# Kernel tuning notes

Measured on AMD Instinct MI355X. Metric: run time of the kernel, lower is better.

Reference implementation:

```python
import jax, jax.numpy as jnp
import numpy as np

BZ, D_IN, D_STATE, D_OUT, L = 8, 256, 512, 256, 4096


def setup_inputs() -> dict:
    key = jax.random.key(0)
    k_u, k_a, k_b, k_c = jax.random.split(key, 4)
    init_scale = 0.5
    u = jax.random.normal(k_u, (BZ, D_IN, L), dtype=jnp.float32)
    A_unconstrained = jax.random.normal(k_a, (D_STATE,), dtype=jnp.float32) * 0.1
    B_mat = jax.random.normal(k_b, (D_STATE, D_IN), dtype=jnp.float32) * init_scale / np.sqrt(D_IN)
    C_mat = jax.random.normal(k_c, (D_OUT, D_STATE), dtype=jnp.float32) * init_scale / np.sqrt(D_STATE)
    D_mat = jnp.zeros((D_OUT, D_IN), dtype=jnp.float32)
    h0 = jnp.zeros((D_STATE,), dtype=jnp.float32)
    return {"u": u, "A_unconstrained": A_unconstrained, "B_mat": B_mat,
            "C_mat": C_mat, "D_mat": D_mat, "h0": h0}


def reference(u, A_unconstrained, B_mat, C_mat, D_mat, h0):
    # u: (B, input_dim, L)
    Bz = u.shape[0]
    A_diag = -jax.nn.softplus(A_unconstrained)          # (S,)
    # Precompute input projection for all timesteps: (L, B, S)
    Bu = jnp.einsum('bil,si->lbs', u, B_mat)
    state0 = jnp.broadcast_to(h0[None, :], (Bz, A_diag.shape[0]))

    def step(state, bu_t):
        x_t = state * A_diag[None, :] + bu_t            # (B, S)
        return x_t, x_t

    _, xs = jax.lax.scan(step, state0, Bu)              # xs: (L, B, S)
    # y_t = x_t @ C^T + u_t @ D^T, assembled as (B, output_dim, L)
    Y = jnp.einsum('lbs,os->bol', xs, C_mat) + jnp.einsum('bil,oi->bol', u, D_mat)
    return Y
```

## Files before the change

### kernel.cpp

```cpp
#include <hip/hip_runtime.h>
#include <math.h>

#define BZ 8
#define DI 256
#define DS 512
#define DOUT 256
#define LL 4096
#define BS (BZ * DS)
#define CH 64
#define CT 64
#define TST 136

typedef __bf16 bf16x8 __attribute__((ext_vector_type(8)));
typedef float f32x4 __attribute__((ext_vector_type(4)));
typedef unsigned short us8 __attribute__((ext_vector_type(8)));

__device__ __forceinline__ ushort f2b(float f) {
    union { float f; unsigned u; } v; v.f = f;
    unsigned r = v.u + 0x7FFFu + ((v.u >> 16) & 1u);
    return (ushort)(r >> 16);
}
__device__ __forceinline__ float b2f(ushort h) {
    union { unsigned u; float f; } v; v.u = ((unsigned)h) << 16;
    return v.f;
}

__device__ __forceinline__ void gload16(const ushort* g, ushort* l) {
    __builtin_amdgcn_global_load_lds(
        (const __attribute__((address_space(1))) unsigned int*)g,
        (__attribute__((address_space(3))) unsigned int*)l,
        16, 0, 0);
}

__global__ __launch_bounds__(256) void k_prep(const float* __restrict__ Au,
                                              float* __restrict__ apow,
                                              const float* __restrict__ Bm,
                                              const float* __restrict__ Cm,
                                              const float* __restrict__ Dm,
                                              ushort* __restrict__ Bmb,
                                              ushort* __restrict__ Cmb,
                                              ushort* __restrict__ Dmb,
                                              int* __restrict__ dflag) {
    const int t = blockIdx.x * 256 + threadIdx.x;
    const int n1 = DS * DI / 4, n2 = DOUT * DS / 4, n3 = DOUT * DI / 4;
    if (t < n1) {
        float4 v = ((const float4*)Bm)[t];
        ushort4 o; o.x = f2b(v.x); o.y = f2b(v.y); o.z = f2b(v.z); o.w = f2b(v.w);
        ((ushort4*)Bmb)[t] = o;
    } else if (t < n1 + n2) {
        float4 v = ((const float4*)Cm)[t - n1];
        ushort4 o; o.x = f2b(v.x); o.y = f2b(v.y); o.z = f2b(v.z); o.w = f2b(v.w);
        ((ushort4*)Cmb)[t - n1] = o;
    } else if (t < n1 + n2 + n3) {
        float4 v = ((const float4*)Dm)[t - n1 - n2];
        ushort4 o; o.x = f2b(v.x); o.y = f2b(v.y); o.z = f2b(v.z); o.w = f2b(v.w);
        ((ushort4*)Dmb)[t - n1 - n2] = o;
        if (v.x != 0.f || v.y != 0.f || v.z != 0.f || v.w != 0.f)
            atomicOr(dflag, 1);
    }
    if (t < DS) {
        float x = Au[t];
        float sp = (x > 15.f) ? x : log1pf(expf(x));
        float ad = -sp;
        float p = 1.f;
        apow[t] = 1.f;
        for (int j = 1; j <= CT; ++j) { p *= ad; apow[j * DS + t] = p; }
    }
}

__global__ __launch_bounds__(256) void k_u2t(const float* __restrict__ u,
                                             ushort* __restrict__ utr) {
    __shared__ float T[64][65];
    const int tid = threadIdx.x;
    const int l0 = blockIdx.x * 64, i0 = blockIdx.y * 64, b = blockIdx.z;
    const int r = tid >> 4, c4 = tid & 15;
#pragma unroll
    for (int rr = r; rr < 64; rr += 16) {
        float4 v = *(const float4*)&u[((size_t)b * DI + i0 + rr) * LL + l0 + c4 * 4];
        T[rr][c4 * 4 + 0] = v.x; T[rr][c4 * 4 + 1] = v.y;
        T[rr][c4 * 4 + 2] = v.z; T[rr][c4 * 4 + 3] = v.w;
    }
    __syncthreads();
#pragma unroll
    for (int ll = r; ll < 64; ll += 16) {
        ushort4 o;
        o.x = f2b(T[c4 * 4 + 0][ll]); o.y = f2b(T[c4 * 4 + 1][ll]);
        o.z = f2b(T[c4 * 4 + 2][ll]); o.w = f2b(T[c4 * 4 + 3][ll]);
        *(ushort4*)&utr[((size_t)b * LL + l0 + ll) * DI + i0 + c4 * 4] = o;
    }
}

__global__ __launch_bounds__(256) void k_bu(const ushort* __restrict__ Bmb,
                                            const ushort* __restrict__ utr,
                                            ushort* __restrict__ Xb,
                                            float* __restrict__ finals,
                                            const float* __restrict__ apow) {
    __shared__ ushort smem[128 * TST];
    const int tid = threadIdx.x;
    const int w = tid >> 6, lane = tid & 63;
    const int l0 = blockIdx.x * 128, s0 = blockIdx.y * 128, b = blockIdx.z;
    const int wm = w & 1, wn = w >> 1;
    const int mrow = lane & 15, quad = lane >> 4;
    const int sr = lane >> 2, sc = (lane & 3) * 8;
    const int off0 = (16 * w) * 32, off1 = (16 * w + 64) * 32;

    f32x4 acc[4][4];
#pragma unroll
    for (int mi = 0; mi < 4; ++mi)
#pragma unroll
        for (int ni = 0; ni < 4; ++ni) acc[mi][ni] = (f32x4)0.f;

    const ushort* ag0 = Bmb + (size_t)(s0 + 16 * w + sr) * DI + sc;
    const ushort* ag1 = ag0 + (size_t)64 * DI;
    const ushort* bg0 = utr + ((size_t)b * LL + l0 + 16 * w + sr) * DI + sc;
    const ushort* bg1 = bg0 + (size_t)64 * DI;

    gload16(ag0, smem + off0); gload16(ag1, smem + off1);
    gload16(bg0, smem + 8192 + off0); gload16(bg1, smem + 8192 + off1);

    for (int it = 0; it < DI / 32; ++it) {
        __syncthreads();
        const int cb = (it & 1) * 4096, nb = 4096 - cb;
        if (it + 1 < DI / 32) {
            const int kk = (it + 1) * 32;
            gload16(ag0 + kk, smem + nb + off0); gload16(ag1 + kk, smem + nb + off1);
            gload16(bg0 + kk, smem + 8192 + nb + off0); gload16(bg1 + kk, smem + 8192 + nb + off1);
        }
        bf16x8 af[4], bfr[4];
#pragma unroll
        for (int mi = 0; mi < 4; ++mi)
            af[mi] = *(const bf16x8*)&smem[cb + (wm * 64 + mi * 16 + mrow) * 32 + quad * 8];
#pragma unroll
        for (int ni = 0; ni < 4; ++ni)
            bfr[ni] = *(const bf16x8*)&smem[8192 + cb + (wn * 64 + ni * 16 + mrow) * 32 + quad * 8];
#pragma unroll
        for (int mi = 0; mi < 4; ++mi)
#pragma unroll
            for (int ni = 0; ni < 4; ++ni)
                acc[mi][ni] = __builtin_amdgcn_mfma_f32_16x16x32_bf16(af[mi], bfr[ni], acc[mi][ni], 0, 0, 0);
    }
    __syncthreads();

#pragma unroll
    for (int mi = 0; mi < 4; ++mi) {
        const int sloc = wm * 64 + mi * 16 + quad * 4;
#pragma unroll
        for (int ni = 0; ni < 4; ++ni) {
            const int lloc = wn * 64 + ni * 16 + mrow;
            f32x4 v = acc[mi][ni];
            ushort4 o; o.x = f2b(v[0]); o.y = f2b(v[1]); o.z = f2b(v[2]); o.w = f2b(v[3]);
            *(ushort4*)&smem[lloc * TST + sloc] = o;
        }
    }
    __syncthreads();
    {
        const int cloc = tid >> 7, sl = tid & 127;
        const float a = apow[DS + s0 + sl];
        float acc2 = 0.f;
        ushort* p = &smem[(cloc * 64) * TST + sl];
#pragma unroll 8
        for (int j = 0; j < CT; ++j) {
            acc2 = a * acc2 + b2f(*p);
            *p = f2b(acc2);
            p += TST;
        }
        finals[(size_t)(l0 / 64 + cloc) * BS + (size_t)b * DS + s0 + sl] = acc2;
    }
    __syncthreads();
    {
        const int rr = tid >> 4, cc = tid & 15;
#pragma unroll
        for (int rep = 0; rep < 8; ++rep) {
            const int l = rep * 16 + rr;
            us8 v = *(const us8*)&smem[l * TST + cc * 8];
            *(us8*)&Xb[(size_t)(l0 + l) * BS + (size_t)b * DS + s0 + cc * 8] = v;
        }
    }
}

__global__ __launch_bounds__(256) void k_carry(const float* __restrict__ finals,
                                               float* __restrict__ carries,
                                               const float* __restrict__ apow,
                                               const float* __restrict__ h0) {
    const int bs = blockIdx.x * 256 + threadIdx.x;
    const int s = bs & (DS - 1);
    const float aT = apow[CT * DS + s];
    float carry = h0[s];
#pragma unroll 8
    for (int c = 0; c < CH; ++c) {
        carries[(size_t)c * BS + bs] = carry;
        carry = aT * carry + finals[(size_t)c * BS + bs];
    }
}

__global__ __launch_bounds__(256) void k_out(const ushort* __restrict__ Cmb,
                                             const ushort* __restrict__ Dmb,
                                             const ushort* __restrict__ Xb,
                                             const ushort* __restrict__ utr,
                                             const float* __restrict__ carries,
                                             const float* __restrict__ apow,
                                             const int* __restrict__ dflag,
                                             float* __restrict__ Y) {
    __shared__ ushort smem[18432];
    const int tid = threadIdx.x;
    const int w = tid >> 6, lane = tid & 63;
    const int l0 = blockIdx.x * 128, o0 = blockIdx.y * 128, b = blockIdx.z;
    const int wm = w & 1, wn = w >> 1;
    const int mrow = lane & 15, quad = lane >> 4;
    const int sr = lane >> 2, sc = (lane & 3) * 8;
    const int off0 = (16 * w) * 32, off1 = (16 * w + 64) * 32;
    const int dnz = *dflag;

    f32x4 acc[4][4];
#pragma unroll
    for (int mi = 0; mi < 4; ++mi)
#pragma unroll
        for (int ni = 0; ni < 4; ++ni) acc[mi][ni] = (f32x4)0.f;

    auto compute = [&](const int aoff, const int ast, const int boff) {
        bf16x8 af[4], bfr[4];
#pragma unroll
        for (int mi = 0; mi < 4; ++mi)
            af[mi] = *(const bf16x8*)&smem[aoff + (wm * 64 + mi * 16 + mrow) * ast + quad * 8];
#pragma unroll
        for (int ni = 0; ni < 4; ++ni)
            bfr[ni] = *(const bf16x8*)&smem[boff + (wn * 64 + ni * 16 + mrow) * 32 + quad * 8];
#pragma unroll
        for (int mi = 0; mi < 4; ++mi)
#pragma unroll
            for (int ni = 0; ni < 4; ++ni)
                acc[mi][ni] = __builtin_amdgcn_mfma_f32_16x16x32_bf16(af[mi], bfr[ni], acc[mi][ni], 0, 0, 0);
    };

    {
        const int r0 = 16 * w + sr;
        const int l_0 = l0 + r0, l_1 = l_0 + 64;
        const int j0 = l_0 & 63, c0 = l_0 >> 6;
        const int j1 = l_1 & 63, c1 = l_1 >> 6;
        const float* ap0 = &apow[(size_t)(j0 + 1) * DS];
        const float* ap1 = &apow[(size_t)(j1 + 1) * DS];
        const float* cr0 = &carries[(size_t)c0 * BS + (size_t)b * DS];
        const float* cr1 = &carries[(size_t)c1 * BS + (size_t)b * DS];
        const ushort* x0 = Xb + (size_t)l_0 * BS + (size_t)b * DS;
        const ushort* x1 = Xb + (size_t)l_1 * BS + (size_t)b * DS;
        const ushort* bg0 = Cmb + (size_t)(o0 + r0) * DS + sc;
        const ushort* bg1 = bg0 + (size_t)64 * DS;

        auto stageA = [&](int it, int dstoff) {
            const int col = it * 32 + sc;
            {
                us8 x = *(const us8*)&x0[col];
                float4 pa = *(const float4*)&ap0[col], pb = *(const float4*)&ap0[col + 4];
                float4 ca = *(const float4*)&cr0[col], cb = *(const float4*)&cr0[col + 4];
                us8 o;
                o[0] = f2b(b2f(x[0]) + pa.x * ca.x); o[1] = f2b(b2f(x[1]) + pa.y * ca.y);
                o[2] = f2b(b2f(x[2]) + pa.z * ca.z); o[3] = f2b(b2f(x[3]) + pa.w * ca.w);
                o[4] = f2b(b2f(x[4]) + pb.x * cb.x); o[5] = f2b(b2f(x[5]) + pb.y * cb.y);
                o[6] = f2b(b2f(x[6]) + pb.z * cb.z); o[7] = f2b(b2f(x[7]) + pb.w * cb.w);
                *(us8*)&smem[dstoff + r0 * 40 + sc] = o;
            }
            {
                us8 x = *(const us8*)&x1[col];
                float4 pa = *(const float4*)&ap1[col], pb = *(const float4*)&ap1[col + 4];
                float4 ca = *(const float4*)&cr1[col], cb = *(const float4*)&cr1[col + 4];
                us8 o;
                o[0] = f2b(b2f(x[0]) + pa.x * ca.x); o[1] = f2b(b2f(x[1]) + pa.y * ca.y);
                o[2] = f2b(b2f(x[2]) + pa.z * ca.z); o[3] = f2b(b2f(x[3]) + pa.w * ca.w);
                o[4] = f2b(b2f(x[4]) + pb.x * cb.x); o[5] = f2b(b2f(x[5]) + pb.y * cb.y);
                o[6] = f2b(b2f(x[6]) + pb.z * cb.z); o[7] = f2b(b2f(x[7]) + pb.w * cb.w);
                *(us8*)&smem[dstoff + (r0 + 64) * 40 + sc] = o;
            }
        };

        stageA(0, 0);
        gload16(bg0, smem + 10240 + off0); gload16(bg1, smem + 10240 + off1);

        for (int it = 0; it < DS / 32; ++it) {
            __syncthreads();
            const int ca_ = (it & 1) * 5120, na_ = 5120 - ca_;
            const int cb_ = 10240 + (it & 1) * 4096, nb_ = 10240 + 4096 - (it & 1) * 4096;
            if (it + 1 < DS / 32) {
                const int kk = (it + 1) * 32;
                gload16(bg0 + kk, smem + nb_ + off0); gload16(bg1 + kk, smem + nb_ + off1);
                stageA(it + 1, na_);
            }
            compute(ca_, 40, cb_);
        }
    }
    if (dnz) {
        const ushort* ag0 = utr + ((size_t)b * LL + l0 + 16 * w + sr) * DI + sc;
        const ushort* ag1 = ag0 + (size_t)64 * DI;
        const ushort* bg0 = Dmb + (size_t)(o0 + 16 * w + sr) * DI + sc;
        const ushort* bg1 = bg0 + (size_t)64 * DI;

        __syncthreads();
        gload16(ag0, smem + off0); gload16(ag1, smem + off1);
        gload16(bg0, smem + 10240 + off0); gload16(bg1, smem + 10240 + off1);

        for (int it = 0; it < DI / 32; ++it) {
            __syncthreads();
            const int ca_ = (it & 1) * 5120, na_ = 5120 - ca_;
            const int cb_ = 10240 + (it & 1) * 4096, nb_ = 10240 + 4096 - (it & 1) * 4096;
            if (it + 1 < DI / 32) {
                const int kk = (it + 1) * 32;
                gload16(ag0 + kk, smem + na_ + off0); gload16(ag1 + kk, smem + na_ + off1);
                gload16(bg0 + kk, smem + nb_ + off0); gload16(bg1 + kk, smem + nb_ + off1);
            }
            compute(ca_, 32, cb_);
        }
    }

#pragma unroll
    for (int mi = 0; mi < 4; ++mi) {
        const int l = l0 + wm * 64 + mi * 16 + quad * 4;
#pragma unroll
        for (int ni = 0; ni < 4; ++ni) {
            const int o = o0 + wn * 64 + ni * 16 + mrow;
            *(float4*)&Y[((size_t)b * DOUT + o) * LL + l] = *(float4*)&acc[mi][ni];
        }
    }
}

extern "C" void kernel_launch(void* const* d_in, const int* in_sizes, int n_in,
                              void* d_out, int out_size, void* d_ws, size_t ws_size,
                              hipStream_t stream) {
    const float* u  = (const float*)d_in[0];
    const float* Au = (const float*)d_in[1];
    const float* Bm = (const float*)d_in[2];
    const float* Cm = (const float*)d_in[3];
    const float* Dm = (const float*)d_in[4];
    const float* h0 = (const float*)d_in[5];
    float* Y = (float*)d_out;

    char* p = (char*)d_ws;
    ushort* utr    = (ushort*)p; p += (size_t)BZ * LL * DI * 2;
    ushort* Xb     = (ushort*)p; p += (size_t)LL * BS * 2;
    float* finals  = (float*)p;  p += (size_t)CH * BS * 4;
    float* carries = (float*)p;  p += (size_t)CH * BS * 4;
    float* apow    = (float*)p;  p += (size_t)(CT + 1) * DS * 4;
    ushort* Bmb    = (ushort*)p; p += (size_t)DS * DI * 2;
    ushort* Cmb    = (ushort*)p; p += (size_t)DOUT * DS * 2;
    ushort* Dmb    = (ushort*)p; p += (size_t)DOUT * DI * 2;
    int* dflag     = (int*)p;    p += 16;

    hipMemsetAsync(dflag, 0, 4, stream);
    k_prep<<<dim3(320), 256, 0, stream>>>(Au, apow, Bm, Cm, Dm, Bmb, Cmb, Dmb, dflag);
    k_u2t<<<dim3(LL / 64, DI / 64, BZ), 256, 0, stream>>>(u, utr);
    k_bu<<<dim3(LL / 128, DS / 128, BZ), 256, 0, stream>>>(Bmb, utr, Xb, finals, apow);
    k_carry<<<dim3(BS / 256), 256, 0, stream>>>(finals, carries, apow, h0);
    k_out<<<dim3(LL / 128, DOUT / 128, BZ), 256, 0, stream>>>(Cmb, Dmb, Xb, utr, carries, apow, dflag, Y);
}
```

Before: 145.4 us.

## Fuse prep into transpose kernel and fold carry scan into output kernel

Merges the weight-conversion/apow prep kernel into the u transpose kernel as extra blocks, and removes the separate carry-scan kernel by having each output block recompute its chunk carries from the per-chunk finals into shared memory. This drops two launches and the carries buffer round trip. In exchange, every k_out block redundantly runs a sequential scan of up to 64 chunks over 512 states, which adds latency before the GEMM starts, especially for blocks handling late chunks.

```diff
diff --git a/kernel.cpp b/kernel.cpp
--- a/kernel.cpp
+++ b/kernel.cpp
@@ -32,61 +32,65 @@
         16, 0, 0);
 }
 
-__global__ __launch_bounds__(256) void k_prep(const float* __restrict__ Au,
-                                              float* __restrict__ apow,
-                                              const float* __restrict__ Bm,
-                                              const float* __restrict__ Cm,
-                                              const float* __restrict__ Dm,
-                                              ushort* __restrict__ Bmb,
-                                              ushort* __restrict__ Cmb,
-                                              ushort* __restrict__ Dmb,
-                                              int* __restrict__ dflag) {
-    const int t = blockIdx.x * 256 + threadIdx.x;
-    const int n1 = DS * DI / 4, n2 = DOUT * DS / 4, n3 = DOUT * DI / 4;
-    if (t < n1) {
-        float4 v = ((const float4*)Bm)[t];
-        ushort4 o; o.x = f2b(v.x); o.y = f2b(v.y); o.z = f2b(v.z); o.w = f2b(v.w);
-        ((ushort4*)Bmb)[t] = o;
-    } else if (t < n1 + n2) {
-        float4 v = ((const float4*)Cm)[t - n1];
-        ushort4 o; o.x = f2b(v.x); o.y = f2b(v.y); o.z = f2b(v.z); o.w = f2b(v.w);
-        ((ushort4*)Cmb)[t - n1] = o;
-    } else if (t < n1 + n2 + n3) {
-        float4 v = ((const float4*)Dm)[t - n1 - n2];
-        ushort4 o; o.x = f2b(v.x); o.y = f2b(v.y); o.z = f2b(v.z); o.w = f2b(v.w);
-        ((ushort4*)Dmb)[t - n1 - n2] = o;
-        if (v.x != 0.f || v.y != 0.f || v.z != 0.f || v.w != 0.f)
-            atomicOr(dflag, 1);
-    }
-    if (t < DS) {
-        float x = Au[t];
-        float sp = (x > 15.f) ? x : log1pf(expf(x));
-        float ad = -sp;
-        float p = 1.f;
-        apow[t] = 1.f;
-        for (int j = 1; j <= CT; ++j) { p *= ad; apow[j * DS + t] = p; }
-    }
-}
-
-__global__ __launch_bounds__(256) void k_u2t(const float* __restrict__ u,
-                                             ushort* __restrict__ utr) {
+__global__ __launch_bounds__(256) void k_prep_u2t(const float* __restrict__ u,
+                                                  ushort* __restrict__ utr,
+                                                  const float* __restrict__ Au,
+                                                  float* __restrict__ apow,
+                                                  const float* __restrict__ Bm,
+                                                  const float* __restrict__ Cm,
+                                                  const float* __restrict__ Dm,
+                                                  ushort* __restrict__ Bmb,
+                                                  ushort* __restrict__ Cmb,
+                                                  ushort* __restrict__ Dmb,
+                                                  int* __restrict__ dflag) {
     __shared__ float T[64][65];
     const int tid = threadIdx.x;
-    const int l0 = blockIdx.x * 64, i0 = blockIdx.y * 64, b = blockIdx.z;
-    const int r = tid >> 4, c4 = tid & 15;
-#pragma unroll
-    for (int rr = r; rr < 64; rr += 16) {
-        float4 v = *(const float4*)&u[((size_t)b * DI + i0 + rr) * LL + l0 + c4 * 4];
-        T[rr][c4 * 4 + 0] = v.x; T[rr][c4 * 4 + 1] = v.y;
-        T[rr][c4 * 4 + 2] = v.z; T[rr][c4 * 4 + 3] = v.w;
-    }
-    __syncthreads();
-#pragma unroll
-    for (int ll = r; ll < 64; ll += 16) {
-        ushort4 o;
-        o.x = f2b(T[c4 * 4 + 0][ll]); o.y = f2b(T[c4 * 4 + 1][ll]);
-        o.z = f2b(T[c4 * 4 + 2][ll]); o.w = f2b(T[c4 * 4 + 3][ll]);
-        *(ushort4*)&utr[((size_t)b * LL + l0 + ll) * DI + i0 + c4 * 4] = o;
+    const int id = blockIdx.x;
+    if (id < 2048) {
+        const int l0 = (id & 63) * 64;
+        const int i0 = ((id >> 6) & 3) * 64;
+        const int b  = id >> 8;
+        const int r = tid >> 4, c4 = tid & 15;
+#pragma unroll
+        for (int rr = r; rr < 64; rr += 16) {
+            float4 v = *(const float4*)&u[((size_t)b * DI + i0 + rr) * LL + l0 + c4 * 4];
+            T[rr][c4 * 4 + 0] = v.x; T[rr][c4 * 4 + 1] = v.y;
+            T[rr][c4 * 4 + 2] = v.z; T[rr][c4 * 4 + 3] = v.w;
+        }
+        __syncthreads();
+#pragma unroll
+        for (int ll = r; ll < 64; ll += 16) {
+            ushort4 o;
+            o.x = f2b(T[c4 * 4 + 0][ll]); o.y = f2b(T[c4 * 4 + 1][ll]);
+            o.z = f2b(T[c4 * 4 + 2][ll]); o.w = f2b(T[c4 * 4 + 3][ll]);
+            *(ushort4*)&utr[((size_t)b * LL + l0 + ll) * DI + i0 + c4 * 4] = o;
+        }
+    } else {
+        const int t = (id - 2048) * 256 + tid;
+        const int n1 = DS * DI / 4, n2 = DOUT * DS / 4, n3 = DOUT * DI / 4;
+        if (t < n1) {
+            float4 v = ((const float4*)Bm)[t];
+            ushort4 o; o.x = f2b(v.x); o.y = f2b(v.y); o.z = f2b(v.z); o.w = f2b(v.w);
+            ((ushort4*)Bmb)[t] = o;
+        } else if (t < n1 + n2) {
+            float4 v = ((const float4*)Cm)[t - n1];
+            ushort4 o; o.x = f2b(v.x); o.y = f2b(v.y); o.z = f2b(v.z); o.w = f2b(v.w);
+            ((ushort4*)Cmb)[t - n1] = o;
+        } else if (t < n1 + n2 + n3) {
+            float4 v = ((const float4*)Dm)[t - n1 - n2];
+            ushort4 o; o.x = f2b(v.x); o.y = f2b(v.y); o.z = f2b(v.z); o.w = f2b(v.w);
+            ((ushort4*)Dmb)[t - n1 - n2] = o;
+            if (v.x != 0.f || v.y != 0.f || v.z != 0.f || v.w != 0.f)
+                atomicOr(dflag, 1);
+        }
+        if (t < DS) {
+            float x = Au[t];
+            float sp = (x > 15.f) ? x : log1pf(expf(x));
+            float ad = -sp;
+            float p = 1.f;
+            apow[t] = 1.f;
+            for (int j = 1; j <= CT; ++j) { p *= ad; apow[j * DS + t] = p; }
+        }
     }
 }
 
@@ -178,30 +182,17 @@
     }
 }
 
-__global__ __launch_bounds__(256) void k_carry(const float* __restrict__ finals,
-                                               float* __restrict__ carries,
-                                               const float* __restrict__ apow,
-                                               const float* __restrict__ h0) {
-    const int bs = blockIdx.x * 256 + threadIdx.x;
-    const int s = bs & (DS - 1);
-    const float aT = apow[CT * DS + s];
-    float carry = h0[s];
-#pragma unroll 8
-    for (int c = 0; c < CH; ++c) {
-        carries[(size_t)c * BS + bs] = carry;
-        carry = aT * carry + finals[(size_t)c * BS + bs];
-    }
-}
-
 __global__ __launch_bounds__(256) void k_out(const ushort* __restrict__ Cmb,
                                              const ushort* __restrict__ Dmb,
                                              const ushort* __restrict__ Xb,
                                              const ushort* __restrict__ utr,
-                                             const float* __restrict__ carries,
+                                             const float* __restrict__ finals,
                                              const float* __restrict__ apow,
+                                             const float* __restrict__ h0,
                                              const int* __restrict__ dflag,
                                              float* __restrict__ Y) {
-    __shared__ ushort smem[18432];
+    __shared__ ushort smem[20480];
+    float* crs = (float*)&smem[18432];
     const int tid = threadIdx.x;
     const int w = tid >> 6, lane = tid & 63;
     const int l0 = blockIdx.x * 128, o0 = blockIdx.y * 128, b = blockIdx.z;
@@ -235,23 +226,35 @@
     {
         const int r0 = 16 * w + sr;
         const int l_0 = l0 + r0, l_1 = l_0 + 64;
-        const int j0 = l_0 & 63, c0 = l_0 >> 6;
-        const int j1 = l_1 & 63, c1 = l_1 >> 6;
+        const int j0 = l_0 & 63;
+        const int j1 = l_1 & 63;
+        const int c0 = l0 >> 6;
         const float* ap0 = &apow[(size_t)(j0 + 1) * DS];
         const float* ap1 = &apow[(size_t)(j1 + 1) * DS];
-        const float* cr0 = &carries[(size_t)c0 * BS + (size_t)b * DS];
-        const float* cr1 = &carries[(size_t)c1 * BS + (size_t)b * DS];
         const ushort* x0 = Xb + (size_t)l_0 * BS + (size_t)b * DS;
         const ushort* x1 = Xb + (size_t)l_1 * BS + (size_t)b * DS;
         const ushort* bg0 = Cmb + (size_t)(o0 + r0) * DS + sc;
         const ushort* bg1 = bg0 + (size_t)64 * DS;
+
+        gload16(bg0, smem + 10240 + off0); gload16(bg1, smem + 10240 + off1);
+
+        for (int s = tid; s < DS; s += 256) {
+            const float aT = apow[CT * DS + s];
+            float carry = h0[s];
+            const float* fb = finals + (size_t)b * DS + s;
+            for (int c = 0; c < c0; ++c)
+                carry = aT * carry + fb[(size_t)c * BS];
+            crs[s] = carry;
+            crs[DS + s] = aT * carry + fb[(size_t)c0 * BS];
+        }
+        __syncthreads();
 
         auto stageA = [&](int it, int dstoff) {
             const int col = it * 32 + sc;
             {
                 us8 x = *(const us8*)&x0[col];
                 float4 pa = *(const float4*)&ap0[col], pb = *(const float4*)&ap0[col + 4];
-                float4 ca = *(const float4*)&cr0[col], cb = *(const float4*)&cr0[col + 4];
+                float4 ca = *(const float4*)&crs[col], cb = *(const float4*)&crs[col + 4];
                 us8 o;
                 o[0] = f2b(b2f(x[0]) + pa.x * ca.x); o[1] = f2b(b2f(x[1]) + pa.y * ca.y);
                 o[2] = f2b(b2f(x[2]) + pa.z * ca.z); o[3] = f2b(b2f(x[3]) + pa.w * ca.w);
@@ -262,7 +265,7 @@
             {
                 us8 x = *(const us8*)&x1[col];
                 float4 pa = *(const float4*)&ap1[col], pb = *(const float4*)&ap1[col + 4];
-                float4 ca = *(const float4*)&cr1[col], cb = *(const float4*)&cr1[col + 4];
+                float4 ca = *(const float4*)&crs[DS + col], cb = *(const float4*)&crs[DS + col + 4];
                 us8 o;
                 o[0] = f2b(b2f(x[0]) + pa.x * ca.x); o[1] = f2b(b2f(x[1]) + pa.y * ca.y);
                 o[2] = f2b(b2f(x[2]) + pa.z * ca.z); o[3] = f2b(b2f(x[3]) + pa.w * ca.w);
@@ -273,7 +276,6 @@
         };
 
         stageA(0, 0);
-        gload16(bg0, smem + 10240 + off0); gload16(bg1, smem + 10240 + off1);
 
         for (int it = 0; it < DS / 32; ++it) {
             __syncthreads();
@@ -336,7 +338,6 @@
     ushort* utr    = (ushort*)p; p += (size_t)BZ * LL * DI * 2;
     ushort* Xb     = (ushort*)p; p += (size_t)LL * BS * 2;
     float* finals  = (float*)p;  p += (size_t)CH * BS * 4;
-    float* carries = (float*)p;  p += (size_t)CH * BS * 4;
     float* apow    = (float*)p;  p += (size_t)(CT + 1) * DS * 4;
     ushort* Bmb    = (ushort*)p; p += (size_t)DS * DI * 2;
     ushort* Cmb    = (ushort*)p; p += (size_t)DOUT * DS * 2;
@@ -344,9 +345,7 @@
     int* dflag     = (int*)p;    p += 16;
 
     hipMemsetAsync(dflag, 0, 4, stream);
-    k_prep<<<dim3(320), 256, 0, stream>>>(Au, apow, Bm, Cm, Dm, Bmb, Cmb, Dmb, dflag);
-    k_u2t<<<dim3(LL / 64, DI / 64, BZ), 256, 0, stream>>>(u, utr);
+    k_prep_u2t<<<dim3(2368), 256, 0, stream>>>(u, utr, Au, apow, Bm, Cm, Dm, Bmb, Cmb, Dmb, dflag);
     k_bu<<<dim3(LL / 128, DS / 128, BZ), 256, 0, stream>>>(Bmb, utr, Xb, finals, apow);
-    k_carry<<<dim3(BS / 256), 256, 0, stream>>>(finals, carries, apow, h0);
-    k_out<<<dim3(LL / 128, DOUT / 128, BZ), 256, 0, stream>>>(Cmb, Dmb, Xb, utr, carries, apow, dflag, Y);
-}
+    k_out<<<dim3(LL / 128, DOUT / 128, BZ), 256, 0, stream>>>(Cmb, Dmb, Xb, utr, finals, apow, h0, dflag, Y);
+}
```

Measured after the change: 160.7 us. 10.5% more time.

## Merge prep and transpose kernels; halve k_out L-tile to 64

Applied to the files above, without the earlier changes.

Fuses the weight-conversion/prep kernel and the u transpose kernel into one launch, dispatching on block index, so one launch and its gap go away. Changes k_out to use 64-row L tiles instead of 128, so each block covers a single chunk and each wave computes a 64x32 output slab. This doubles the grid, lowers LDS and register use per block to raise occupancy, and simplifies the carry-correction staging. In exchange, the C and D matrix tiles are reloaded twice as often across blocks.

```diff
diff --git a/kernel.cpp b/kernel.cpp
--- a/kernel.cpp
+++ b/kernel.cpp
@@ -32,61 +32,65 @@
         16, 0, 0);
 }
 
-__global__ __launch_bounds__(256) void k_prep(const float* __restrict__ Au,
-                                              float* __restrict__ apow,
-                                              const float* __restrict__ Bm,
-                                              const float* __restrict__ Cm,
-                                              const float* __restrict__ Dm,
-                                              ushort* __restrict__ Bmb,
-                                              ushort* __restrict__ Cmb,
-                                              ushort* __restrict__ Dmb,
-                                              int* __restrict__ dflag) {
-    const int t = blockIdx.x * 256 + threadIdx.x;
-    const int n1 = DS * DI / 4, n2 = DOUT * DS / 4, n3 = DOUT * DI / 4;
-    if (t < n1) {
-        float4 v = ((const float4*)Bm)[t];
-        ushort4 o; o.x = f2b(v.x); o.y = f2b(v.y); o.z = f2b(v.z); o.w = f2b(v.w);
-        ((ushort4*)Bmb)[t] = o;
-    } else if (t < n1 + n2) {
-        float4 v = ((const float4*)Cm)[t - n1];
-        ushort4 o; o.x = f2b(v.x); o.y = f2b(v.y); o.z = f2b(v.z); o.w = f2b(v.w);
-        ((ushort4*)Cmb)[t - n1] = o;
-    } else if (t < n1 + n2 + n3) {
-        float4 v = ((const float4*)Dm)[t - n1 - n2];
-        ushort4 o; o.x = f2b(v.x); o.y = f2b(v.y); o.z = f2b(v.z); o.w = f2b(v.w);
-        ((ushort4*)Dmb)[t - n1 - n2] = o;
-        if (v.x != 0.f || v.y != 0.f || v.z != 0.f || v.w != 0.f)
-            atomicOr(dflag, 1);
-    }
-    if (t < DS) {
-        float x = Au[t];
-        float sp = (x > 15.f) ? x : log1pf(expf(x));
-        float ad = -sp;
-        float p = 1.f;
-        apow[t] = 1.f;
-        for (int j = 1; j <= CT; ++j) { p *= ad; apow[j * DS + t] = p; }
-    }
-}
-
-__global__ __launch_bounds__(256) void k_u2t(const float* __restrict__ u,
-                                             ushort* __restrict__ utr) {
+__global__ __launch_bounds__(256) void k_prep_u2t(const float* __restrict__ u,
+                                                  ushort* __restrict__ utr,
+                                                  const float* __restrict__ Au,
+                                                  float* __restrict__ apow,
+                                                  const float* __restrict__ Bm,
+                                                  const float* __restrict__ Cm,
+                                                  const float* __restrict__ Dm,
+                                                  ushort* __restrict__ Bmb,
+                                                  ushort* __restrict__ Cmb,
+                                                  ushort* __restrict__ Dmb,
+                                                  int* __restrict__ dflag) {
     __shared__ float T[64][65];
     const int tid = threadIdx.x;
-    const int l0 = blockIdx.x * 64, i0 = blockIdx.y * 64, b = blockIdx.z;
-    const int r = tid >> 4, c4 = tid & 15;
-#pragma unroll
-    for (int rr = r; rr < 64; rr += 16) {
-        float4 v = *(const float4*)&u[((size_t)b * DI + i0 + rr) * LL + l0 + c4 * 4];
-        T[rr][c4 * 4 + 0] = v.x; T[rr][c4 * 4 + 1] = v.y;
-        T[rr][c4 * 4 + 2] = v.z; T[rr][c4 * 4 + 3] = v.w;
-    }
-    __syncthreads();
-#pragma unroll
-    for (int ll = r; ll < 64; ll += 16) {
-        ushort4 o;
-        o.x = f2b(T[c4 * 4 + 0][ll]); o.y = f2b(T[c4 * 4 + 1][ll]);
-        o.z = f2b(T[c4 * 4 + 2][ll]); o.w = f2b(T[c4 * 4 + 3][ll]);
-        *(ushort4*)&utr[((size_t)b * LL + l0 + ll) * DI + i0 + c4 * 4] = o;
+    const int id = blockIdx.x;
+    if (id < 2048) {
+        const int l0 = (id & 63) * 64;
+        const int i0 = ((id >> 6) & 3) * 64;
+        const int b  = id >> 8;
+        const int r = tid >> 4, c4 = tid & 15;
+#pragma unroll
+        for (int rr = r; rr < 64; rr += 16) {
+            float4 v = *(const float4*)&u[((size_t)b * DI + i0 + rr) * LL + l0 + c4 * 4];
+            T[rr][c4 * 4 + 0] = v.x; T[rr][c4 * 4 + 1] = v.y;
+            T[rr][c4 * 4 + 2] = v.z; T[rr][c4 * 4 + 3] = v.w;
+        }
+        __syncthreads();
+#pragma unroll
+        for (int ll = r; ll < 64; ll += 16) {
+            ushort4 o;
+            o.x = f2b(T[c4 * 4 + 0][ll]); o.y = f2b(T[c4 * 4 + 1][ll]);
+            o.z = f2b(T[c4 * 4 + 2][ll]); o.w = f2b(T[c4 * 4 + 3][ll]);
+            *(ushort4*)&utr[((size_t)b * LL + l0 + ll) * DI + i0 + c4 * 4] = o;
+        }
+    } else {
+        const int t = (id - 2048) * 256 + tid;
+        const int n1 = DS * DI / 4, n2 = DOUT * DS / 4, n3 = DOUT * DI / 4;
+        if (t < n1) {
+            float4 v = ((const float4*)Bm)[t];
+            ushort4 o; o.x = f2b(v.x); o.y = f2b(v.y); o.z = f2b(v.z); o.w = f2b(v.w);
+            ((ushort4*)Bmb)[t] = o;
+        } else if (t < n1 + n2) {
+            float4 v = ((const float4*)Cm)[t - n1];
+            ushort4 o; o.x = f2b(v.x); o.y = f2b(v.y); o.z = f2b(v.z); o.w = f2b(v.w);
+            ((ushort4*)Cmb)[t - n1] = o;
+        } else if (t < n1 + n2 + n3) {
+            float4 v = ((const float4*)Dm)[t - n1 - n2];
+            ushort4 o; o.x = f2b(v.x); o.y = f2b(v.y); o.z = f2b(v.z); o.w = f2b(v.w);
+            ((ushort4*)Dmb)[t - n1 - n2] = o;
+            if (v.x != 0.f || v.y != 0.f || v.z != 0.f || v.w != 0.f)
+                atomicOr(dflag, 1);
+        }
+        if (t < DS) {
+            float x = Au[t];
+            float sp = (x > 15.f) ? x : log1pf(expf(x));
+            float ad = -sp;
+            float p = 1.f;
+            apow[t] = 1.f;
+            for (int j = 1; j <= CT; ++j) { p *= ad; apow[j * DS + t] = p; }
+        }
     }
 }
 
@@ -201,84 +205,65 @@
                                              const float* __restrict__ apow,
                                              const int* __restrict__ dflag,
                                              float* __restrict__ Y) {
-    __shared__ ushort smem[18432];
+    __shared__ ushort smem[13312];
     const int tid = threadIdx.x;
     const int w = tid >> 6, lane = tid & 63;
-    const int l0 = blockIdx.x * 128, o0 = blockIdx.y * 128, b = blockIdx.z;
-    const int wm = w & 1, wn = w >> 1;
+    const int l0 = blockIdx.x * 64, o0 = blockIdx.y * 128, b = blockIdx.z;
     const int mrow = lane & 15, quad = lane >> 4;
     const int sr = lane >> 2, sc = (lane & 3) * 8;
     const int off0 = (16 * w) * 32, off1 = (16 * w + 64) * 32;
     const int dnz = *dflag;
 
-    f32x4 acc[4][4];
+    f32x4 acc[4][2];
 #pragma unroll
     for (int mi = 0; mi < 4; ++mi)
 #pragma unroll
-        for (int ni = 0; ni < 4; ++ni) acc[mi][ni] = (f32x4)0.f;
+        for (int ni = 0; ni < 2; ++ni) acc[mi][ni] = (f32x4)0.f;
 
     auto compute = [&](const int aoff, const int ast, const int boff) {
-        bf16x8 af[4], bfr[4];
+        bf16x8 af[4], bfr[2];
 #pragma unroll
         for (int mi = 0; mi < 4; ++mi)
-            af[mi] = *(const bf16x8*)&smem[aoff + (wm * 64 + mi * 16 + mrow) * ast + quad * 8];
-#pragma unroll
-        for (int ni = 0; ni < 4; ++ni)
-            bfr[ni] = *(const bf16x8*)&smem[boff + (wn * 64 + ni * 16 + mrow) * 32 + quad * 8];
+            af[mi] = *(const bf16x8*)&smem[aoff + (mi * 16 + mrow) * ast + quad * 8];
+#pragma unroll
+        for (int ni = 0; ni < 2; ++ni)
+            bfr[ni] = *(const bf16x8*)&smem[boff + (32 * w + ni * 16 + mrow) * 32 + quad * 8];
 #pragma unroll
         for (int mi = 0; mi < 4; ++mi)
 #pragma unroll
-            for (int ni = 0; ni < 4; ++ni)
+            for (int ni = 0; ni < 2; ++ni)
                 acc[mi][ni] = __builtin_amdgcn_mfma_f32_16x16x32_bf16(af[mi], bfr[ni], acc[mi][ni], 0, 0, 0);
     };
 
     {
         const int r0 = 16 * w + sr;
-        const int l_0 = l0 + r0, l_1 = l_0 + 64;
-        const int j0 = l_0 & 63, c0 = l_0 >> 6;
-        const int j1 = l_1 & 63, c1 = l_1 >> 6;
-        const float* ap0 = &apow[(size_t)(j0 + 1) * DS];
-        const float* ap1 = &apow[(size_t)(j1 + 1) * DS];
+        const int c0 = l0 >> 6;
+        const float* ap0 = &apow[(size_t)(r0 + 1) * DS];
         const float* cr0 = &carries[(size_t)c0 * BS + (size_t)b * DS];
-        const float* cr1 = &carries[(size_t)c1 * BS + (size_t)b * DS];
-        const ushort* x0 = Xb + (size_t)l_0 * BS + (size_t)b * DS;
-        const ushort* x1 = Xb + (size_t)l_1 * BS + (size_t)b * DS;
+        const ushort* x0 = Xb + (size_t)(l0 + r0) * BS + (size_t)b * DS;
         const ushort* bg0 = Cmb + (size_t)(o0 + r0) * DS + sc;
         const ushort* bg1 = bg0 + (size_t)64 * DS;
 
         auto stageA = [&](int it, int dstoff) {
             const int col = it * 32 + sc;
-            {
-                us8 x = *(const us8*)&x0[col];
-                float4 pa = *(const float4*)&ap0[col], pb = *(const float4*)&ap0[col + 4];
-                float4 ca = *(const float4*)&cr0[col], cb = *(const float4*)&cr0[col + 4];
-                us8 o;
-                o[0] = f2b(b2f(x[0]) + pa.x * ca.x); o[1] = f2b(b2f(x[1]) + pa.y * ca.y);
-                o[2] = f2b(b2f(x[2]) + pa.z * ca.z); o[3] = f2b(b2f(x[3]) + pa.w * ca.w);
-                o[4] = f2b(b2f(x[4]) + pb.x * cb.x); o[5] = f2b(b2f(x[5]) + pb.y * cb.y);
-                o[6] = f2b(b2f(x[6]) + pb.z * cb.z); o[7] = f2b(b2f(x[7]) + pb.w * cb.w);
-                *(us8*)&smem[dstoff + r0 * 40 + sc] = o;
-            }
-            {
-                us8 x = *(const us8*)&x1[col];
-                float4 pa = *(const float4*)&ap1[col], pb = *(const float4*)&ap1[col + 4];
-                float4 ca = *(const float4*)&cr1[col], cb = *(const float4*)&cr1[col + 4];
-                us8 o;
-                o[0] = f2b(b2f(x[0]) + pa.x * ca.x); o[1] = f2b(b2f(x[1]) + pa.y * ca.y);
-                o[2] = f2b(b2f(x[2]) + pa.z * ca.z); o[3] = f2b(b2f(x[3]) + pa.w * ca.w);
-                o[4] = f2b(b2f(x[4]) + pb.x * cb.x); o[5] = f2b(b2f(x[5]) + pb.y * cb.y);
-                o[6] = f2b(b2f(x[6]) + pb.z * cb.z); o[7] = f2b(b2f(x[7]) + pb.w * cb.w);
-                *(us8*)&smem[dstoff + (r0 + 64) * 40 + sc] = o;
-            }
+            us8 x = *(const us8*)&x0[col];
+            float4 pa = *(const float4*)&ap0[col], pb = *(const float4*)&ap0[col + 4];
+            float4 ca = *(const float4*)&cr0[col], cb = *(const float4*)&cr0[col + 4];
+            us8 o;
+            o[0] = f2b(b2f(x[0]) + pa.x * ca.x); o[1] = f2b(b2f(x[1]) + pa.y * ca.y);
+            o[2] = f2b(b2f(x[2]) + pa.z * ca.z); o[3] = f2b(b2f(x[3]) + pa.w * ca.w);
+            o[4] = f2b(b2f(x[4]) + pb.x * cb.x); o[5] = f2b(b2f(x[5]) + pb.y * cb.y);
+            o[6] = f2b(b2f(x[6]) + pb.z * cb.z); o[7] = f2b(b2f(x[7]) + pb.w * cb.w);
+            *(us8*)&smem[dstoff + r0 * 40 + sc] = o;
         };
 
         stageA(0, 0);
-        gload16(bg0, smem + 10240 + off0); gload16(bg1, smem + 10240 + off1);
+        gload16(bg0, smem + 5120 + off0); gload16(bg1, smem + 5120 + off1);
 
         for (int it = 0; it < DS / 32; ++it) {
             __syncthreads();
-            const int ca_ = (it & 1) * 5120, na_ = 5120 - ca_;
-            const int cb_ = 10240 + (it & 1) * 4096, nb_ = 10240 + 4096 - (it & 1) * 4096;
+            const int ca_ = (it & 1) * 2560, na_ = 2560 - ca_;
+            const int cb_ = 5120 + (it & 1) * 4096, nb_ = 5120 + 4096 - (it & 1) * 4096;
             if (it + 1 < DS / 32) {
                 const int kk = (it + 1) * 32;
                 gload16(bg0 + kk, smem + nb_ + off0); gload16(bg1 + kk, smem + nb_ + off1);
@@ -289,21 +274,20 @@
     }
     if (dnz) {
         const ushort* ag0 = utr + ((size_t)b * LL + l0 + 16 * w + sr) * DI + sc;
-        const ushort* ag1 = ag0 + (size_t)64 * DI;
         const ushort* bg0 = Dmb + (size_t)(o0 + 16 * w + sr) * DI + sc;
         const ushort* bg1 = bg0 + (size_t)64 * DI;
 
         __syncthreads();
-        gload16(ag0, smem + off0); gload16(ag1, smem + off1);
-        gload16(bg0, smem + 10240 + off0); gload16(bg1, smem + 10240 + off1);
+        gload16(ag0, smem + off0);
+        gload16(bg0, smem + 5120 + off0); gload16(bg1, smem + 5120 + off1);
 
         for (int it = 0; it < DI / 32; ++it) {
             __syncthreads();
-            const int ca_ = (it & 1) * 5120, na_ = 5120 - ca_;
-            const int cb_ = 10240 + (it & 1) * 4096, nb_ = 10240 + 4096 - (it & 1) * 4096;
+            const int ca_ = (it & 1) * 2560, na_ = 2560 - ca_;
+            const int cb_ = 5120 + (it & 1) * 4096, nb_ = 5120 + 4096 - (it & 1) * 4096;
             if (it + 1 < DI / 32) {
                 const int kk = (it + 1) * 32;
-                gload16(ag0 + kk, smem + na_ + off0); gload16(ag1 + kk, smem + na_ + off1);
+                gload16(ag0 + kk, smem + na_ + off0);
                 gload16(bg0 + kk, smem + nb_ + off0); gload16(bg1 + kk, smem + nb_ + off1);
             }
             compute(ca_, 32, cb_);
@@ -312,10 +296,10 @@
 
 #pragma unroll
     for (int mi = 0; mi < 4; ++mi) {
-        const int l = l0 + wm * 64 + mi * 16 + quad * 4;
-#pragma unroll
-        for (int ni = 0; ni < 4; ++ni) {
-            const int o = o0 + wn * 64 + ni * 16 + mrow;
+        const int l = l0 + mi * 16 + quad * 4;
+#pragma unroll
+        for (int ni = 0; ni < 2; ++ni) {
+            const int o = o0 + 32 * w + ni * 16 + mrow;
             *(float4*)&Y[((size_t)b * DOUT + o) * LL + l] = *(float4*)&acc[mi][ni];
         }
     }
@@ -344,9 +328,8 @@
     int* dflag     = (int*)p;    p += 16;
 
     hipMemsetAsync(dflag, 0, 4, stream);
-    k_prep<<<dim3(320), 256, 0, stream>>>(Au, apow, Bm, Cm, Dm, Bmb, Cmb, Dmb, dflag);
-    k_u2t<<<dim3(LL / 64, DI / 64, BZ), 256, 0, stream>>>(u, utr);
+    k_prep_u2t<<<dim3(2368), 256, 0, stream>>>(u, utr, Au, apow, Bm, Cm, Dm, Bmb, Cmb, Dmb, dflag);
     k_bu<<<dim3(LL / 128, DS / 128, BZ), 256, 0, stream>>>(Bmb, utr, Xb, finals, apow);
     k_carry<<<dim3(BS / 256), 256, 0, stream>>>(finals, carries, apow, h0);
-    k_out<<<dim3(LL / 128, DOUT / 128, BZ), 256, 0, stream>>>(Cmb, Dmb, Xb, utr, carries, apow, dflag, Y);
-}
+    k_out<<<dim3(LL / 64, DOUT / 128, BZ), 256, 0, stream>>>(Cmb, Dmb, Xb, utr, carries, apow, dflag, Y);
+}
```

Result: no change. 146.0 us (+0.4%).
